# Performance work log

Measured on AMD Instinct MI355X. Metric: run time of the kernel, lower is better.

## Reference

```python
import jax, jax.numpy as jnp
import numpy as np

B, T, E, H, DL, CC, K = 64, 2048, 512, 128, 1024, 32, 31


def setup_inputs() -> dict:
    key = jax.random.key(0)
    ks = jax.random.split(key, 8)
    return {
        "encoder_output": jax.random.normal(ks[0], (B, T, E), jnp.float32),
        "processed_encoder_output": jax.random.normal(ks[1], (B, T, H), jnp.float32),
        "lstm_output": jax.random.normal(ks[2], (B, 1, DL), jnp.float32),
        "attention_weights_cum": jax.random.uniform(ks[3], (B, T), jnp.float32),
        # learned params (torch Linear stores [out, in]; y = x @ W.T)
        "W_lstm": jax.random.normal(ks[4], (H, DL), jnp.float32) * 0.02,
        "conv_w": jax.random.normal(ks[5], (CC, 1, K), jnp.float32) * 0.1,
        "W_loc": jax.random.normal(ks[6], (H, CC), jnp.float32) * 0.1,
        "W_e": jax.random.normal(ks[7], (1, H), jnp.float32) * 0.1,
    }


def _forward(encoder_output, processed_encoder_output, lstm_output,
             attention_weights_cum, W_lstm, conv_w, W_loc, W_e):
    # [B,1,1024] @ [1024,128] -> [B,1,128]
    processed_lstm = jnp.einsum('bqd,hd->bqh', lstm_output, W_lstm)
    # location conv: [B,1,T] -> [B,32,T], same padding
    loc = lax.conv_general_dilated(
        attention_weights_cum[:, None, :], conv_w,
        window_strides=(1,), padding=[(K // 2, K // 2)],
        dimension_numbers=('NCH', 'OIH', 'NCH'))
    # transpose to [B,T,32] then dense to [B,T,128]
    processed_attn = jnp.einsum('bct,hc->bth', loc, W_loc)
    # additive energies: [B,T,128] -> [B,T]
    energies = jnp.einsum('bth,oh->bto',
                          jnp.tanh(processed_lstm + processed_attn + processed_encoder_output),
                          W_e)[..., 0]
    attention_weights = jax.nn.softmax(energies, axis=1)  # [B,T]
    # bmm: [B,1,T] @ [B,T,E] -> [B,1,E]
    attention_context = jnp.einsum('bt,bte->be', attention_weights, encoder_output)[:, None, :]
    return attention_context, attention_weights

from jax import lax


def reference(encoder_output, processed_encoder_output, lstm_output,
              attention_weights_cum, W_lstm, conv_w, W_loc, W_e):
    return _forward(encoder_output, processed_encoder_output, lstm_output,
                    attention_weights_cum, W_lstm, conv_w, W_loc, W_e)
```

## Files before the change

### kernel.cpp

```cpp
#include <hip/hip_runtime.h>
#include <math.h>


#define BB 64
#define TT 2048
#define EE 512
#define HH 128
#define DLL 1024
#define CCC 32
#define KK 31

#define WS_FW   0
#define WS_PL   4096
#define WS_EN   12288
#define WS_ST   143360
#define WS_PART 145472

__global__ __launch_bounds__(256) void k0_prep(const float* __restrict__ lstm,
                                               const float* __restrict__ Wl,
                                               const float* __restrict__ cw,
                                               const float* __restrict__ Wloc,
                                               float* __restrict__ ws) {
  const int blk = blockIdx.x;
  const int tid = threadIdx.x;
  if (blk < 2048) {
    const int wave = tid >> 6, lane = tid & 63;
    const int wg = blk * 4 + wave;
    const int b = wg >> 7, h = wg & 127;
    const float4* wr = (const float4*)(Wl + (size_t)h * DLL);
    const float4* lr = (const float4*)(lstm + (size_t)b * DLL);
    float s = 0.f;
#pragma unroll
    for (int m = 0; m < 4; ++m) {
      float4 a = wr[m * 64 + lane];
      float4 c = lr[m * 64 + lane];
      s += a.x * c.x + a.y * c.y + a.z * c.z + a.w * c.w;
    }
#pragma unroll
    for (int m = 1; m < 64; m <<= 1) s += __shfl_xor(s, m, 64);
    if (lane == 0) ws[WS_PL + b * HH + h] = s;
  } else {
    __shared__ __align__(16) float wl_s[HH * CCC];
    __shared__ __align__(16) float cw_s[CCC * KK];
#pragma unroll
    for (int m = 0; m < 4; ++m)
      ((float4*)wl_s)[tid + 256 * m] = ((const float4*)Wloc)[tid + 256 * m];
    if (tid < 248) ((float4*)cw_s)[tid] = ((const float4*)cw)[tid];
    __syncthreads();
    const int h = tid >> 1;
    const int kbase = (tid & 1) * 16;
    const int kn = (tid & 1) ? 15 : 16;
    for (int kk = 0; kk < kn; ++kk) {
      const int k = kbase + kk;
      float s = 0.f;
#pragma unroll
      for (int c = 0; c < CCC; ++c) s += wl_s[h * CCC + c] * cw_s[c * KK + k];
      ws[WS_FW + h * 32 + k] = s;
    }
    if (tid & 1) ws[WS_FW + h * 32 + 31] = 0.f;
  }
}

__global__ __launch_bounds__(128) void k1_fused(const float* __restrict__ pe,
                                                const float* __restrict__ aw,
                                                const float* __restrict__ We,
                                                const float* __restrict__ enc,
                                                float* __restrict__ ws) {
  const int b = blockIdx.y;
  const int chunk = blockIdx.x;
  const int t0 = chunk * 128;
  const int tid = threadIdx.x;
  const int wave = tid >> 6, lane = tid & 63;

  __shared__ __align__(16) float fw_s[HH * 32];
  __shared__ __align__(16) float aw_s[160];
  __shared__ float pl_s[128];
  __shared__ float we_s[128];
  __shared__ float w_chunk[128];
  __shared__ float sm[2], ss[2];

  {
    const float4* src = (const float4*)(ws + WS_FW);
    float4* dst = (float4*)fw_s;
#pragma unroll
    for (int i = 0; i < 8; ++i) dst[tid + 128 * i] = src[tid + 128 * i];
  }
  {
    int tg = t0 - 16 + tid;
    aw_s[tid] = (tg >= 0 && tg < TT) ? aw[b * TT + tg] : 0.f;
    if (tid < 32) {
      tg = t0 + 112 + tid;
      aw_s[128 + tid] = (tg >= 0 && tg < TT) ? aw[b * TT + tg] : 0.f;
    }
  }
  pl_s[tid] = ws[WS_PL + b * HH + tid];
  we_s[tid] = We[tid];
  __syncthreads();

  float wreg[32];
#pragma unroll
  for (int k = 0; k < 32; ++k) wreg[k] = aw_s[tid + 1 + k];

  const float4* pr4 = (const float4*)(pe + ((size_t)b * TT + t0 + tid) * HH);
  float e_acc = 0.f;

#pragma unroll 1
  for (int h0 = 0; h0 < 128; h0 += 16) {
    float4 ptv[4];
#pragma unroll
    for (int i = 0; i < 4; ++i) ptv[i] = pr4[(h0 >> 2) + i];
    float pts[16];
#pragma unroll
    for (int i = 0; i < 4; ++i) {
      pts[4 * i + 0] = ptv[i].x; pts[4 * i + 1] = ptv[i].y;
      pts[4 * i + 2] = ptv[i].z; pts[4 * i + 3] = ptv[i].w;
    }
#pragma unroll 2
    for (int hh = 0; hh < 16; ++hh) {
      const int h = h0 + hh;
      const float4* fr = (const float4*)&fw_s[h * 32];
      float a0 = pl_s[h] + pts[hh];
      float a1 = 0.f;
#pragma unroll
      for (int q = 0; q < 8; ++q) {
        const float4 f = fr[q];
        a0 = fmaf(f.x, wreg[4 * q + 0], a0);
        a1 = fmaf(f.y, wreg[4 * q + 1], a1);
        a0 = fmaf(f.z, wreg[4 * q + 2], a0);
        a1 = fmaf(f.w, wreg[4 * q + 3], a1);
      }
      const float x = a0 + a1;
      const float th = 1.f - 2.f / (__expf(2.f * x) + 1.f);
      e_acc = fmaf(we_s[h], th, e_acc);
    }
  }

  ws[WS_EN + b * TT + t0 + tid] = e_acc;

  float m = e_acc;
#pragma unroll
  for (int s = 1; s < 64; s <<= 1) m = fmaxf(m, __shfl_xor(m, s, 64));
  float p = __expf(e_acc - m);
#pragma unroll
  for (int s = 1; s < 64; s <<= 1) p += __shfl_xor(p, s, 64);
  if (lane == 0) { sm[wave] = m; ss[wave] = p; }
  __syncthreads();
  const float mb = fmaxf(sm[0], sm[1]);
  if (tid == 0) {
    const float sb = ss[0] * __expf(sm[0] - mb) + ss[1] * __expf(sm[1] - mb);
    float* st = ws + WS_ST + (b * 16 + chunk) * 2;
    st[0] = mb;
    st[1] = sb;
  }
  w_chunk[tid] = __expf(e_acc - mb);
  __syncthreads();

  const float4* enc4 = (const float4*)(enc + ((size_t)b * TT + t0) * EE);
  float4 acc0 = {0.f, 0.f, 0.f, 0.f}, acc1 = {0.f, 0.f, 0.f, 0.f};
#pragma unroll 8
  for (int t = 0; t < 128; ++t) {
    const float w = w_chunk[t];
    const float4 v = enc4[(size_t)t * 128 + tid];
    if (t & 1) {
      acc1.x = fmaf(w, v.x, acc1.x); acc1.y = fmaf(w, v.y, acc1.y);
      acc1.z = fmaf(w, v.z, acc1.z); acc1.w = fmaf(w, v.w, acc1.w);
    } else {
      acc0.x = fmaf(w, v.x, acc0.x); acc0.y = fmaf(w, v.y, acc0.y);
      acc0.z = fmaf(w, v.z, acc0.z); acc0.w = fmaf(w, v.w, acc0.w);
    }
  }
  acc0.x += acc1.x; acc0.y += acc1.y; acc0.z += acc1.z; acc0.w += acc1.w;
  ((float4*)(ws + WS_PART))[(size_t)(b * 16 + chunk) * 128 + tid] = acc0;
}

__global__ __launch_bounds__(256) void k2_combine(const float* __restrict__ ws,
                                                  float* __restrict__ wts,
                                                  float* __restrict__ ctx) {
  const int b = blockIdx.x;
  const int tid = threadIdx.x;

  const float* st = ws + WS_ST + b * 32;
  float mb = -3.4e38f;
#pragma unroll
  for (int c = 0; c < 16; ++c) mb = fmaxf(mb, st[2 * c]);
  float S = 0.f;
#pragma unroll
  for (int c = 0; c < 16; ++c) S += st[2 * c + 1] * __expf(st[2 * c] - mb);
  const float inv = 1.f / S;

  __shared__ float esc[16];
  if (tid < 16) esc[tid] = __expf(st[2 * tid] - mb) * inv;
  __syncthreads();

  const float4* en4 = (const float4*)(ws + WS_EN + (size_t)b * TT);
  float4* w4 = (float4*)(wts + (size_t)b * TT);
#pragma unroll
  for (int j = 0; j < 2; ++j) {
    const float4 e = en4[tid * 2 + j];
    float4 w;
    w.x = __expf(e.x - mb) * inv;
    w.y = __expf(e.y - mb) * inv;
    w.z = __expf(e.z - mb) * inv;
    w.w = __expf(e.w - mb) * inv;
    w4[tid * 2 + j] = w;
  }

  const float2* p2 = (const float2*)(ws + WS_PART) + (size_t)b * 16 * 256 + tid;
  float2 s = {0.f, 0.f};
#pragma unroll
  for (int c = 0; c < 16; ++c) {
    const float2 v = p2[c * 256];
    s.x = fmaf(esc[c], v.x, s.x);
    s.y = fmaf(esc[c], v.y, s.y);
  }
  ((float2*)ctx)[b * 256 + tid] = s;
}

extern "C" void kernel_launch(void* const* d_in, const int* in_sizes, int n_in,
                              void* d_out, int out_size, void* d_ws, size_t ws_size,
                              hipStream_t stream) {
  const float* enc  = (const float*)d_in[0];
  const float* pe   = (const float*)d_in[1];
  const float* lstm = (const float*)d_in[2];
  const float* awc  = (const float*)d_in[3];
  const float* Wl   = (const float*)d_in[4];
  const float* cw   = (const float*)d_in[5];
  const float* Wloc = (const float*)d_in[6];
  const float* We   = (const float*)d_in[7];

  float* out = (float*)d_out;
  float* ctx = out;
  float* wts = out + BB * EE;
  float* ws = (float*)d_ws;

  k0_prep<<<2049, 256, 0, stream>>>(lstm, Wl, cw, Wloc, ws);
  k1_fused<<<dim3(16, BB), 128, 0, stream>>>(pe, awc, We, enc, ws);
  k2_combine<<<BB, 256, 0, stream>>>(ws, wts, ctx);
}
```

Measured before the change: 86.50 us.

## Warp-specialize fused attention kernel: producer waves compute energies, consumers stream encoder

Each block now covers 256 timesteps with 256 threads. Two waves compute energies and per-64-step softmax stats in four sub-chunks and publish each one through LDS flags. The other two waves spin on those flags and accumulate the encoder-weighted context with an online rescaled max as each sub-chunk arrives. The aim is to overlap the tanh/energy compute with the bandwidth-bound encoder stream, and halve the number of partials the combine kernel merges. In exchange there are fewer blocks, fewer waves issuing encoder loads, and spin-wait overhead on the consumer side.

```diff
diff --git a/kernel.cpp b/kernel.cpp
--- a/kernel.cpp
+++ b/kernel.cpp
@@ -14,7 +14,7 @@
 #define WS_PL   4096
 #define WS_EN   12288
 #define WS_ST   143360
-#define WS_PART 145472
+#define WS_PART 144384
 
 __global__ __launch_bounds__(256) void k0_prep(const float* __restrict__ lstm,
                                                const float* __restrict__ Wl,
@@ -61,116 +61,143 @@
   }
 }
 
-__global__ __launch_bounds__(128) void k1_fused(const float* __restrict__ pe,
+__global__ __launch_bounds__(256) void k1_fused(const float* __restrict__ pe,
                                                 const float* __restrict__ aw,
                                                 const float* __restrict__ We,
                                                 const float* __restrict__ enc,
                                                 float* __restrict__ ws) {
   const int b = blockIdx.y;
   const int chunk = blockIdx.x;
-  const int t0 = chunk * 128;
+  const int t0 = chunk * 256;
   const int tid = threadIdx.x;
   const int wave = tid >> 6, lane = tid & 63;
 
   __shared__ __align__(16) float fw_s[HH * 32];
-  __shared__ __align__(16) float aw_s[160];
+  __shared__ __align__(16) float aw_s[288];
   __shared__ float pl_s[128];
   __shared__ float we_s[128];
-  __shared__ float w_chunk[128];
-  __shared__ float sm[2], ss[2];
+  __shared__ float w_s[256];
+  __shared__ float m_arr[4], s_arr[4];
+  __shared__ int flag_s[4];
 
   {
     const float4* src = (const float4*)(ws + WS_FW);
     float4* dst = (float4*)fw_s;
 #pragma unroll
-    for (int i = 0; i < 8; ++i) dst[tid + 128 * i] = src[tid + 128 * i];
+    for (int i = 0; i < 4; ++i) dst[tid + 256 * i] = src[tid + 256 * i];
   }
   {
     int tg = t0 - 16 + tid;
     aw_s[tid] = (tg >= 0 && tg < TT) ? aw[b * TT + tg] : 0.f;
     if (tid < 32) {
-      tg = t0 + 112 + tid;
-      aw_s[128 + tid] = (tg >= 0 && tg < TT) ? aw[b * TT + tg] : 0.f;
-    }
-  }
-  pl_s[tid] = ws[WS_PL + b * HH + tid];
-  we_s[tid] = We[tid];
+      tg = t0 + 240 + tid;
+      aw_s[256 + tid] = (tg >= 0 && tg < TT) ? aw[b * TT + tg] : 0.f;
+    }
+  }
+  if (tid < 128) {
+    pl_s[tid] = ws[WS_PL + b * HH + tid];
+    we_s[tid] = We[tid];
+  }
+  if (tid < 4) flag_s[tid] = 0;
   __syncthreads();
 
-  float wreg[32];
-#pragma unroll
-  for (int k = 0; k < 32; ++k) wreg[k] = aw_s[tid + 1 + k];
-
-  const float4* pr4 = (const float4*)(pe + ((size_t)b * TT + t0 + tid) * HH);
-  float e_acc = 0.f;
-
+  if (wave < 2) {
+    for (int si = 0; si < 2; ++si) {
+      const int sub = si * 2 + wave;
+      const int lt = sub * 64 + lane;
+      float wreg[32];
+#pragma unroll
+      for (int k = 0; k < 32; ++k) wreg[k] = aw_s[lt + 1 + k];
+      const float4* pr4 = (const float4*)(pe + ((size_t)b * TT + t0 + lt) * HH);
+      float e_acc = 0.f;
 #pragma unroll 1
-  for (int h0 = 0; h0 < 128; h0 += 16) {
-    float4 ptv[4];
-#pragma unroll
-    for (int i = 0; i < 4; ++i) ptv[i] = pr4[(h0 >> 2) + i];
-    float pts[16];
-#pragma unroll
-    for (int i = 0; i < 4; ++i) {
-      pts[4 * i + 0] = ptv[i].x; pts[4 * i + 1] = ptv[i].y;
-      pts[4 * i + 2] = ptv[i].z; pts[4 * i + 3] = ptv[i].w;
-    }
+      for (int h0 = 0; h0 < 128; h0 += 16) {
+        float4 ptv[4];
+#pragma unroll
+        for (int i = 0; i < 4; ++i) ptv[i] = pr4[(h0 >> 2) + i];
+        float pts[16];
+#pragma unroll
+        for (int i = 0; i < 4; ++i) {
+          pts[4 * i + 0] = ptv[i].x; pts[4 * i + 1] = ptv[i].y;
+          pts[4 * i + 2] = ptv[i].z; pts[4 * i + 3] = ptv[i].w;
+        }
 #pragma unroll 2
-    for (int hh = 0; hh < 16; ++hh) {
-      const int h = h0 + hh;
-      const float4* fr = (const float4*)&fw_s[h * 32];
-      float a0 = pl_s[h] + pts[hh];
-      float a1 = 0.f;
-#pragma unroll
-      for (int q = 0; q < 8; ++q) {
-        const float4 f = fr[q];
-        a0 = fmaf(f.x, wreg[4 * q + 0], a0);
-        a1 = fmaf(f.y, wreg[4 * q + 1], a1);
-        a0 = fmaf(f.z, wreg[4 * q + 2], a0);
-        a1 = fmaf(f.w, wreg[4 * q + 3], a1);
+        for (int hh = 0; hh < 16; ++hh) {
+          const int h = h0 + hh;
+          const float4* fr = (const float4*)&fw_s[h * 32];
+          float a0 = pl_s[h] + pts[hh];
+          float a1 = 0.f;
+#pragma unroll
+          for (int q = 0; q < 8; ++q) {
+            const float4 f = fr[q];
+            a0 = fmaf(f.x, wreg[4 * q + 0], a0);
+            a1 = fmaf(f.y, wreg[4 * q + 1], a1);
+            a0 = fmaf(f.z, wreg[4 * q + 2], a0);
+            a1 = fmaf(f.w, wreg[4 * q + 3], a1);
+          }
+          const float x = a0 + a1;
+          const float th = 1.f - 2.f / (__expf(2.f * x) + 1.f);
+          e_acc = fmaf(we_s[h], th, e_acc);
+        }
       }
-      const float x = a0 + a1;
-      const float th = 1.f - 2.f / (__expf(2.f * x) + 1.f);
-      e_acc = fmaf(we_s[h], th, e_acc);
-    }
-  }
-
-  ws[WS_EN + b * TT + t0 + tid] = e_acc;
-
-  float m = e_acc;
-#pragma unroll
-  for (int s = 1; s < 64; s <<= 1) m = fmaxf(m, __shfl_xor(m, s, 64));
-  float p = __expf(e_acc - m);
-#pragma unroll
-  for (int s = 1; s < 64; s <<= 1) p += __shfl_xor(p, s, 64);
-  if (lane == 0) { sm[wave] = m; ss[wave] = p; }
+      ws[WS_EN + b * TT + t0 + lt] = e_acc;
+
+      float m = e_acc;
+#pragma unroll
+      for (int s = 1; s < 64; s <<= 1) m = fmaxf(m, __shfl_xor(m, s, 64));
+      float p = __expf(e_acc - m);
+#pragma unroll
+      for (int s = 1; s < 64; s <<= 1) p += __shfl_xor(p, s, 64);
+      w_s[lt] = __expf(e_acc - m);
+      if (lane == 0) { m_arr[sub] = m; s_arr[sub] = p; }
+      __hip_atomic_store(&flag_s[sub], 1, __ATOMIC_RELEASE,
+                         __HIP_MEMORY_SCOPE_WORKGROUP);
+    }
+  } else {
+    const int col = tid & 127;
+    const float4* enc4 = (const float4*)(enc + ((size_t)b * TT + t0) * EE);
+    float4 a0 = {0.f, 0.f, 0.f, 0.f}, a1 = {0.f, 0.f, 0.f, 0.f};
+    float mrun = -3.4e38f;
+#pragma unroll 1
+    for (int sub = 0; sub < 4; ++sub) {
+      while (!__hip_atomic_load(&flag_s[sub], __ATOMIC_ACQUIRE,
+                                __HIP_MEMORY_SCOPE_WORKGROUP))
+        __builtin_amdgcn_s_sleep(2);
+      const float mi = m_arr[sub];
+      const float mnew = fmaxf(mrun, mi);
+      const float so = __expf(mrun - mnew);
+      const float sc = __expf(mi - mnew);
+      a0.x *= so; a0.y *= so; a0.z *= so; a0.w *= so;
+      a1.x *= so; a1.y *= so; a1.z *= so; a1.w *= so;
+      const float* wp = &w_s[sub * 64];
+#pragma unroll 8
+      for (int t = 0; t < 64; ++t) {
+        const float w = wp[t] * sc;
+        const float4 v = enc4[(size_t)(sub * 64 + t) * 128 + col];
+        if (t & 1) {
+          a1.x = fmaf(w, v.x, a1.x); a1.y = fmaf(w, v.y, a1.y);
+          a1.z = fmaf(w, v.z, a1.z); a1.w = fmaf(w, v.w, a1.w);
+        } else {
+          a0.x = fmaf(w, v.x, a0.x); a0.y = fmaf(w, v.y, a0.y);
+          a0.z = fmaf(w, v.z, a0.z); a0.w = fmaf(w, v.w, a0.w);
+        }
+      }
+      mrun = mnew;
+    }
+    a0.x += a1.x; a0.y += a1.y; a0.z += a1.z; a0.w += a1.w;
+    ((float4*)(ws + WS_PART))[(size_t)(b * 8 + chunk) * 128 + col] = a0;
+  }
+
   __syncthreads();
-  const float mb = fmaxf(sm[0], sm[1]);
   if (tid == 0) {
-    const float sb = ss[0] * __expf(sm[0] - mb) + ss[1] * __expf(sm[1] - mb);
-    float* st = ws + WS_ST + (b * 16 + chunk) * 2;
+    const float mb = fmaxf(fmaxf(m_arr[0], m_arr[1]), fmaxf(m_arr[2], m_arr[3]));
+    float sb = 0.f;
+#pragma unroll
+    for (int c = 0; c < 4; ++c) sb += s_arr[c] * __expf(m_arr[c] - mb);
+    float* st = ws + WS_ST + (b * 8 + chunk) * 2;
     st[0] = mb;
     st[1] = sb;
   }
-  w_chunk[tid] = __expf(e_acc - mb);
-  __syncthreads();
-
-  const float4* enc4 = (const float4*)(enc + ((size_t)b * TT + t0) * EE);
-  float4 acc0 = {0.f, 0.f, 0.f, 0.f}, acc1 = {0.f, 0.f, 0.f, 0.f};
-#pragma unroll 8
-  for (int t = 0; t < 128; ++t) {
-    const float w = w_chunk[t];
-    const float4 v = enc4[(size_t)t * 128 + tid];
-    if (t & 1) {
-      acc1.x = fmaf(w, v.x, acc1.x); acc1.y = fmaf(w, v.y, acc1.y);
-      acc1.z = fmaf(w, v.z, acc1.z); acc1.w = fmaf(w, v.w, acc1.w);
-    } else {
-      acc0.x = fmaf(w, v.x, acc0.x); acc0.y = fmaf(w, v.y, acc0.y);
-      acc0.z = fmaf(w, v.z, acc0.z); acc0.w = fmaf(w, v.w, acc0.w);
-    }
-  }
-  acc0.x += acc1.x; acc0.y += acc1.y; acc0.z += acc1.z; acc0.w += acc1.w;
-  ((float4*)(ws + WS_PART))[(size_t)(b * 16 + chunk) * 128 + tid] = acc0;
 }
 
 __global__ __launch_bounds__(256) void k2_combine(const float* __restrict__ ws,
@@ -179,17 +206,17 @@
   const int b = blockIdx.x;
   const int tid = threadIdx.x;
 
-  const float* st = ws + WS_ST + b * 32;
+  const float* st = ws + WS_ST + b * 16;
   float mb = -3.4e38f;
 #pragma unroll
-  for (int c = 0; c < 16; ++c) mb = fmaxf(mb, st[2 * c]);
+  for (int c = 0; c < 8; ++c) mb = fmaxf(mb, st[2 * c]);
   float S = 0.f;
 #pragma unroll
-  for (int c = 0; c < 16; ++c) S += st[2 * c + 1] * __expf(st[2 * c] - mb);
+  for (int c = 0; c < 8; ++c) S += st[2 * c + 1] * __expf(st[2 * c] - mb);
   const float inv = 1.f / S;
 
-  __shared__ float esc[16];
-  if (tid < 16) esc[tid] = __expf(st[2 * tid] - mb) * inv;
+  __shared__ float esc[8];
+  if (tid < 8) esc[tid] = __expf(st[2 * tid] - mb) * inv;
   __syncthreads();
 
   const float4* en4 = (const float4*)(ws + WS_EN + (size_t)b * TT);
@@ -205,10 +232,10 @@
     w4[tid * 2 + j] = w;
   }
 
-  const float2* p2 = (const float2*)(ws + WS_PART) + (size_t)b * 16 * 256 + tid;
+  const float2* p2 = (const float2*)(ws + WS_PART) + (size_t)b * 8 * 256 + tid;
   float2 s = {0.f, 0.f};
 #pragma unroll
-  for (int c = 0; c < 16; ++c) {
+  for (int c = 0; c < 8; ++c) {
     const float2 v = p2[c * 256];
     s.x = fmaf(esc[c], v.x, s.x);
     s.y = fmaf(esc[c], v.y, s.y);
@@ -234,6 +261,6 @@
   float* ws = (float*)d_ws;
 
   k0_prep<<<2049, 256, 0, stream>>>(lstm, Wl, cw, Wloc, ws);
-  k1_fused<<<dim3(16, BB), 128, 0, stream>>>(pe, awc, We, enc, ws);
+  k1_fused<<<dim3(8, BB), 256, 0, stream>>>(pe, awc, We, enc, ws);
   k2_combine<<<BB, 256, 0, stream>>>(ws, wts, ctx);
 }
```

Result: slower. 112.7 us (+30.4%).
